# Optimization experiments

Measured on AMD Instinct MI355X. Metric: run time of the kernel, lower is better.

Reference implementation:

```python
import jax, jax.numpy as jnp
import numpy as np

EMBED = 128
HEADS = 32          # embed_dim // 4, forced by fuse Conv2d channel counts
HEAD_DIM = EMBED // HEADS  # 4
WS = (4, 7, 7)
N = WS[0] * WS[1] * WS[2]  # 196 tokens per window
B = 64              # batch * num_windows
SCALE = HEAD_DIM ** -0.5
EPS = 1e-5


def _rel_index():
    d, h, w = WS
    coords = np.stack(np.meshgrid(np.arange(d), np.arange(h), np.arange(w), indexing='ij'))
    flat = coords.reshape(3, -1)                       # [3, N]
    rel = (flat[:, :, None] - flat[:, None, :]).transpose(1, 2, 0).astype(np.int64)  # [N,N,3]
    rel[:, :, 0] += d - 1
    rel[:, :, 1] += h - 1
    rel[:, :, 2] += w - 1
    rel[:, :, 0] *= (2 * h - 1) * (2 * w - 1)
    rel[:, :, 1] *= (2 * w - 1)
    return rel.sum(-1).astype(np.int32)                # [N, N]


def setup_inputs() -> dict:
    key = jax.random.key(0)
    ks = jax.random.split(key, 7)
    d, h, w = WS
    tbl = (2 * d - 1) * (2 * h - 1) * (2 * w - 1)
    return {
        'x_in':      jax.random.normal(ks[0], (B, N, EMBED), dtype=jnp.float32),
        'x_in2':     jax.random.normal(ks[1], (B, N, EMBED), dtype=jnp.float32),
        'qkv_w':     jax.random.normal(ks[2], (3 * EMBED, EMBED), dtype=jnp.float32) * 0.02,
        'proj_w':    jax.random.normal(ks[3], (EMBED, EMBED), dtype=jnp.float32) * 0.02,
        'proj_b':    jnp.zeros((EMBED,), dtype=jnp.float32),
        'rpb_table': jax.random.normal(ks[4], (tbl, HEADS), dtype=jnp.float32) * 0.02,
        'fuse_w':    jax.random.normal(ks[5], (EMBED // 4, EMBED // 2), dtype=jnp.float32) * 0.1,
        'fuse_b':    jnp.zeros((EMBED // 4,), dtype=jnp.float32),
        'rel_idx':   jnp.asarray(_rel_index()),
    }


def _branch(x, qkv_w):
    b, n, c = x.shape
    qkv = (x @ qkv_w.T).reshape(b, n, 3, HEADS, c // HEADS).transpose(2, 0, 3, 1, 4)
    q, k, v = qkv[0] * SCALE, qkv[1], qkv[2]           # [b, H, n, d]
    attn = jnp.einsum('bhnd,bhmd->bhnm', q, k)         # [b, H, n, n]
    return attn, v


def reference(x_in, x_in2, qkv_w, proj_w, proj_b, rpb_table, fuse_w, fuse_b, rel_idx):
    b, n, c = x_in.shape
    attn1, v1 = _branch(x_in, qkv_w)
    attn2, v2 = _branch(x_in2, qkv_w)

    # conv-gated value fusion: Conv2d 1x1 over channel dim (= 2H) + InstanceNorm2d + ReLU + Sigmoid
    vcat = jnp.concatenate([v1, v2], axis=1)           # [b, 2H, n, d]
    v = jnp.einsum('bcnd,oc->bond', vcat, fuse_w) + fuse_b[None, :, None, None]  # [b, H, n, d]
    mu = v.mean(axis=(2, 3), keepdims=True)
    var = v.var(axis=(2, 3), keepdims=True)            # biased, as InstanceNorm2d
    v = (v - mu) * jax.lax.rsqrt(var + EPS)
    v = jax.nn.sigmoid(jax.nn.relu(v))

    # relative position bias: gather [n*n] rows of table -> [H, n, n]
    bias = rpb_table[rel_idx[:n, :n].reshape(-1)].reshape(n, n, HEADS).transpose(2, 0, 1)

    attn = jax.nn.softmax(attn1 + attn2 + bias[None], axis=-1)  # [b, H, n, n]
    x = jnp.einsum('bhnm,bhmd->bhnd', attn, v).transpose(0, 2, 1, 3).reshape(b, n, c)
    return x @ proj_w.T + proj_b
```

## Files before the change

kernel.cpp:

```cpp
#include <hip/hip_runtime.h>
#include <hip/hip_bf16.h>
#include <stdint.h>

#define NB   64
#define NTOK 196
#define NH   32
#define HD   4
#define CE   128
#define NM   38416

typedef __bf16 bf16x8 __attribute__((ext_vector_type(8)));
typedef short  bf16x4s __attribute__((ext_vector_type(4)));
typedef float  f32x4  __attribute__((ext_vector_type(4)));

#define QSCALE 0.7213475204444817f
#define LOG2E  1.4426950408889634f

__device__ __forceinline__ float u2f(unsigned short u) {
    union { unsigned int i; float f; } z;
    z.i = ((unsigned int)u) << 16;
    return z.f;
}
__device__ __forceinline__ unsigned short f2u(float f) {
    union { float f; unsigned int i; } z; z.f = f;
    unsigned int x = z.i;
    return (unsigned short)((x + 0x7fffu + ((x >> 16) & 1u)) >> 16);
}

extern "C" __global__ __launch_bounds__(256) void qkv_bias(
    const float* __restrict__ x1,
    const float* __restrict__ x2,
    const float* __restrict__ qkvw,
    const int* __restrict__ rel_idx, const float* __restrict__ rpb,
    unsigned short* __restrict__ Qb, unsigned short* __restrict__ Kb,
    unsigned short* __restrict__ V, unsigned short* __restrict__ biasM)
{
    __shared__ alignas(16) unsigned short AT[64][136];
    __shared__ alignas(16) unsigned short BT[64][136];
    const int tid = threadIdx.x;

    if (blockIdx.y == 6) {
        const int bx = blockIdx.x;
        const int qt = bx % 13, h = bx / 13;
        const int lane = tid & 63, wv = tid >> 6;
        const int quad = lane >> 4, tc = lane & 15;
        for (int nt = wv; nt < 14; nt += 4) {
            union { uint2 v; unsigned short s[4]; } e;
#pragma unroll
            for (int r = 0; r < 4; ++r) {
                int q   = qt * 16 + tc;
                int key = nt * 16 + quad * 4 + r;
                unsigned short u = 0xFF80;
                if (q < 196 && key < 196) {
                    int idx = rel_idx[q * 196 + key];
                    u = f2u(rpb[idx * 32 + h] * LOG2E);
                }
                e.s[r] = u;
            }
            unsigned int off = (((h * 13 + qt) * 7 + (nt >> 1)) * 64 + lane) * 8
                               + (nt & 1) * 4;
            *(uint2*)(biasM + off) = e.v;
        }
        return;
    }
    if (blockIdx.x >= 392) return;

    const int r0 = blockIdx.x * 64;
    const int j0 = blockIdx.y * 64;

    for (int idx = tid; idx < 2048; idx += 256) {
        int row = idx >> 5, k0 = (idx & 31) << 2;
        int r = r0 + row;
        const float* xp = (r >= 12544) ? x2 : x1;
        int rem = r - ((r >= 12544) ? 12544 : 0);
        float4 v = *(const float4*)&xp[rem * 128 + k0];
        ushort4 u; u.x = f2u(v.x); u.y = f2u(v.y); u.z = f2u(v.z); u.w = f2u(v.w);
        *(ushort4*)&AT[row][k0] = u;
    }
    for (int idx = tid; idx < 2048; idx += 256) {
        int row = idx >> 5, k0 = (idx & 31) << 2;
        float4 v = *(const float4*)&qkvw[(j0 + row) * 128 + k0];
        ushort4 u; u.x = f2u(v.x); u.y = f2u(v.y); u.z = f2u(v.z); u.w = f2u(v.w);
        *(ushort4*)&BT[row][k0] = u;
    }
    __syncthreads();

    const int lane = tid & 63, w = tid >> 6;
    const int wj = (w >> 1) * 32;
    const int wt = (w & 1) * 32;
    const int quad = lane >> 4, tc = lane & 15;

    f32x4 acc[2][2] = {};
#pragma unroll
    for (int ks = 0; ks < 4; ++ks) {
        int k0 = ks * 32 + quad * 8;
        bf16x8 a0 = *(const bf16x8*)&BT[wj + tc][k0];
        bf16x8 a1 = *(const bf16x8*)&BT[wj + 16 + tc][k0];
        bf16x8 b0 = *(const bf16x8*)&AT[wt + tc][k0];
        bf16x8 b1 = *(const bf16x8*)&AT[wt + 16 + tc][k0];
        acc[0][0] = __builtin_amdgcn_mfma_f32_16x16x32_bf16(a0, b0, acc[0][0], 0, 0, 0);
        acc[0][1] = __builtin_amdgcn_mfma_f32_16x16x32_bf16(a0, b1, acc[0][1], 0, 0, 0);
        acc[1][0] = __builtin_amdgcn_mfma_f32_16x16x32_bf16(a1, b0, acc[1][0], 0, 0, 0);
        acc[1][1] = __builtin_amdgcn_mfma_f32_16x16x32_bf16(a1, b1, acc[1][1], 0, 0, 0);
    }

    const int sel = j0 >> 7;
#pragma unroll
    for (int mi = 0; mi < 2; ++mi) {
        int jbase = (j0 + wj + mi * 16 + quad * 4) & 127;
        int hh = jbase >> 2;
#pragma unroll
        for (int ni = 0; ni < 2; ++ni) {
            int tok = r0 + wt + ni * 16 + tc;
            int branch = (tok >= 12544) ? 1 : 0;
            int rem = tok - branch * 12544;
            int bb = rem / 196;
            int nn = rem - bb * 196;
            union { uint2 v; unsigned short s[4]; } pk2;
            if (sel == 0) {
#pragma unroll
                for (int r = 0; r < 4; ++r) pk2.s[r] = f2u(acc[mi][ni][r] * QSCALE);
                *(uint2*)&Qb[((bb * 32 + hh) * 196 + nn) * 8 + branch * 4] = pk2.v;
            } else if (sel == 1) {
#pragma unroll
                for (int r = 0; r < 4; ++r) pk2.s[r] = f2u(acc[mi][ni][r]);
                *(uint2*)&Kb[((bb * 32 + hh) * 196 + nn) * 8 + branch * 4] = pk2.v;
            } else {
#pragma unroll
                for (int r = 0; r < 4; ++r) pk2.s[r] = f2u(acc[mi][ni][r]);
                *(uint2*)&V[(bb * 64 + branch * 32 + hh) * 784 + nn * 4] = pk2.v;
            }
        }
    }
}

__device__ __forceinline__ float block_sum(float v, float* red, int tid) {
#pragma unroll
    for (int off = 32; off > 0; off >>= 1) v += __shfl_down(v, off);
    __syncthreads();
    if ((tid & 63) == 0) red[tid >> 6] = v;
    __syncthreads();
    return red[0] + red[1] + red[2] + red[3];
}

__device__ __forceinline__ float act_sig_relu(float x) {
    return x > 0.f ? __fdividef(1.f, 1.f + __expf(-x)) : 0.5f;
}

extern "C" __global__ __launch_bounds__(256) void fuse_kernel(
    const unsigned short* __restrict__ V,
    const float* __restrict__ fuse_w,
    const float* __restrict__ fuse_b,
    float* __restrict__ Vf)
{
    const int b = blockIdx.x, o0 = blockIdx.y * 2;
    const int tid = threadIdx.x;
    __shared__ float fws[2][64];
    __shared__ float red[4];
    if (tid < 128) fws[tid >> 6][tid & 63] = fuse_w[(o0 + (tid >> 6)) * 64 + (tid & 63)];
    __syncthreads();

    const unsigned short* Vb = V + b * 64 * 784;
    float a0[3] = {0.f, 0.f, 0.f}, a1[3] = {0.f, 0.f, 0.f};
    float t0 = 0.f, t1 = 0.f;
    const bool tail = tid < 16;
    for (int c = 0; c < 64; ++c) {
        float w0 = fws[0][c], w1 = fws[1][c];
        const unsigned short* Vc = Vb + c * 784;
#pragma unroll
        for (int k = 0; k < 3; ++k) {
            float x = u2f(Vc[tid + 256 * k]);
            a0[k] = fmaf(w0, x, a0[k]);
            a1[k] = fmaf(w1, x, a1[k]);
        }
        if (tail) {
            float x = u2f(Vc[tid + 768]);
            t0 = fmaf(w0, x, t0);
            t1 = fmaf(w1, x, t1);
        }
    }
    float fb0 = fuse_b[o0], fb1 = fuse_b[o0 + 1];
#pragma unroll
    for (int k = 0; k < 3; ++k) { a0[k] += fb0; a1[k] += fb1; }
    t0 += fb0; t1 += fb1;

    float s0 = a0[0] + a0[1] + a0[2] + (tail ? t0 : 0.f);
    float q0 = a0[0]*a0[0] + a0[1]*a0[1] + a0[2]*a0[2] + (tail ? t0*t0 : 0.f);
    float s1 = a1[0] + a1[1] + a1[2] + (tail ? t1 : 0.f);
    float q1 = a1[0]*a1[0] + a1[1]*a1[1] + a1[2]*a1[2] + (tail ? t1*t1 : 0.f);

    float S0 = block_sum(s0, red, tid);
    float Q0 = block_sum(q0, red, tid);
    float S1 = block_sum(s1, red, tid);
    float Q1 = block_sum(q1, red, tid);

    const float inv = 1.0f / 784.0f;
    float mu0 = S0 * inv, mu1 = S1 * inv;
    float rs0 = rsqrtf(Q0 * inv - mu0 * mu0 + 1e-5f);
    float rs1 = rsqrtf(Q1 * inv - mu1 * mu1 + 1e-5f);

    float* out0 = Vf + (b * 32 + o0) * 784;
    float* out1 = out0 + 784;
#pragma unroll
    for (int k = 0; k < 3; ++k) {
        int e = tid + 256 * k;
        out0[e] = act_sig_relu((a0[k] - mu0) * rs0);
        out1[e] = act_sig_relu((a1[k] - mu1) * rs1);
    }
    if (tail) {
        out0[tid + 768] = act_sig_relu((t0 - mu0) * rs0);
        out1[tid + 768] = act_sig_relu((t1 - mu1) * rs1);
    }
}

extern "C" __global__ __launch_bounds__(256) void attn_kernel(
    const unsigned short* __restrict__ Qb, const unsigned short* __restrict__ Kb,
    const float* __restrict__ Vf, const unsigned short* __restrict__ biasM,
    unsigned short* __restrict__ Ob)
{
    const int bh = blockIdx.x;
    const int b = bh >> 5, h = bh & 31;
    __shared__ alignas(16) unsigned short Qs[208][8];
    __shared__ alignas(16) unsigned short Ks[224][8];
    __shared__ alignas(16) unsigned short VT[16][232];
    const int tid = threadIdx.x;

    const unsigned short* Qrow = Qb + bh * 196 * 8;
    const unsigned short* Krow = Kb + bh * 196 * 8;
    if (tid < 208) {
        uint4 z = {0, 0, 0, 0};
        uint4 v = (tid < 196) ? *(const uint4*)(Qrow + tid * 8) : z;
        *(uint4*)&Qs[tid][0] = v;
    }
    if (tid < 224) {
        uint4 z = {0, 0, 0, 0};
        uint4 v = (tid < 196) ? *(const uint4*)(Krow + tid * 8) : z;
        *(uint4*)&Ks[tid][0] = v;
    }
    {
        unsigned int* vtw = (unsigned int*)&VT[0][0];
        for (int i = tid; i < (16 * 232) / 2; i += 256) vtw[i] = 0u;
    }
    __syncthreads();
    if (tid < 196) {
        float4 vv = *(const float4*)(Vf + bh * 784 + tid * 4);
        VT[0][tid] = f2u(vv.x); VT[1][tid] = f2u(vv.y);
        VT[2][tid] = f2u(vv.z); VT[3][tid] = f2u(vv.w);
        VT[4][tid] = 0x3F80;
    }
    __syncthreads();

    const int lane = tid & 63, wv = tid >> 6;
    const int quad = lane >> 4, tc = lane & 15;

    bf16x4s vfr16[14];
#pragma unroll
    for (int t = 0; t < 14; ++t)
        vfr16[t] = *(const bf16x4s*)&VT[tc][t * 16 + quad * 4];

    const unsigned short* bias_h = biasM + (unsigned)(h * 13) * 3584;

    for (int qt = wv; qt < 13; qt += 4) {
        bf16x8 bq = {};
        if (quad == 0) bq = *(const bf16x8*)&Qs[qt * 16 + tc][0];
        const unsigned short* bias_q = bias_h + qt * 3584;
        f32x4 Oacc = {};
#pragma unroll
        for (int kt = 0; kt < 7; ++kt) {
            uint4 bw = *(const uint4*)(bias_q + kt * 512 + lane * 8);
            f32x4 s0, s1;
            {
                union { unsigned int u; float f; } c;
                c.u = bw.x << 16;          s0[0] = c.f;
                c.u = bw.x & 0xffff0000u;  s0[1] = c.f;
                c.u = bw.y << 16;          s0[2] = c.f;
                c.u = bw.y & 0xffff0000u;  s0[3] = c.f;
                c.u = bw.z << 16;          s1[0] = c.f;
                c.u = bw.z & 0xffff0000u;  s1[1] = c.f;
                c.u = bw.w << 16;          s1[2] = c.f;
                c.u = bw.w & 0xffff0000u;  s1[3] = c.f;
            }
            bf16x8 a0 = *(const bf16x8*)&Ks[(kt * 2 + 0) * 16 + tc][0];
            bf16x8 a1 = *(const bf16x8*)&Ks[(kt * 2 + 1) * 16 + tc][0];
            s0 = __builtin_amdgcn_mfma_f32_16x16x32_bf16(a0, bq, s0, 0, 0, 0);
            s1 = __builtin_amdgcn_mfma_f32_16x16x32_bf16(a1, bq, s1, 0, 0, 0);
            float e0 = __builtin_amdgcn_exp2f(s0[0]);
            float e1 = __builtin_amdgcn_exp2f(s0[1]);
            float e2 = __builtin_amdgcn_exp2f(s0[2]);
            float e3 = __builtin_amdgcn_exp2f(s0[3]);
            float g0 = __builtin_amdgcn_exp2f(s1[0]);
            float g1 = __builtin_amdgcn_exp2f(s1[1]);
            float g2 = __builtin_amdgcn_exp2f(s1[2]);
            float g3 = __builtin_amdgcn_exp2f(s1[3]);
            union { int d[2]; bf16x4s v; } pf0, pf1;
            pf0.d[0] = (int)__builtin_amdgcn_perm(__float_as_uint(e1), __float_as_uint(e0), 0x07060302u);
            pf0.d[1] = (int)__builtin_amdgcn_perm(__float_as_uint(e3), __float_as_uint(e2), 0x07060302u);
            pf1.d[0] = (int)__builtin_amdgcn_perm(__float_as_uint(g1), __float_as_uint(g0), 0x07060302u);
            pf1.d[1] = (int)__builtin_amdgcn_perm(__float_as_uint(g3), __float_as_uint(g2), 0x07060302u);
            Oacc = __builtin_amdgcn_mfma_f32_16x16x16bf16_1k(vfr16[kt * 2 + 0], pf0.v, Oacc, 0, 0, 0);
            Oacc = __builtin_amdgcn_mfma_f32_16x16x16bf16_1k(vfr16[kt * 2 + 1], pf1.v, Oacc, 0, 0, 0);
        }
        float rs = __shfl(Oacc[0], 16 + tc);
        int q = qt * 16 + tc;
        if (quad == 0 && q < 196) {
            float inv = __builtin_amdgcn_rcpf(rs);
            union { uint2 v; unsigned short s[4]; } pk2;
            pk2.s[0] = f2u(Oacc[0] * inv);
            pk2.s[1] = f2u(Oacc[1] * inv);
            pk2.s[2] = f2u(Oacc[2] * inv);
            pk2.s[3] = f2u(Oacc[3] * inv);
            *(uint2*)&Ob[(b * 196 + q) * 128 + h * 4] = pk2.v;
        }
    }
}

extern "C" __global__ __launch_bounds__(256) void proj_kernel(
    const unsigned short* __restrict__ Ob, const float* __restrict__ projw,
    const float* __restrict__ projb, float* __restrict__ out)
{
    __shared__ alignas(16) unsigned short AT[64][136];
    __shared__ alignas(16) unsigned short BT[64][136];
    const int tid = threadIdx.x;
    const int r0 = blockIdx.x * 64;
    const int j0 = blockIdx.y * 64;

    for (int idx = tid; idx < 1024; idx += 256) {
        int row = idx >> 4, k0 = (idx & 15) << 3;
        *(uint4*)&AT[row][k0] = *(const uint4*)&Ob[(r0 + row) * 128 + k0];
    }
    for (int idx = tid; idx < 2048; idx += 256) {
        int row = idx >> 5, k0 = (idx & 31) << 2;
        float4 v = *(const float4*)&projw[(j0 + row) * 128 + k0];
        ushort4 u; u.x = f2u(v.x); u.y = f2u(v.y); u.z = f2u(v.z); u.w = f2u(v.w);
        *(ushort4*)&BT[row][k0] = u;
    }
    __syncthreads();

    const int lane = tid & 63, w = tid >> 6;
    const int wm = (w >> 1) * 32, wn = (w & 1) * 32;
    const int quad = lane >> 4, tcol = lane & 15;

    f32x4 acc[2][2] = {};
#pragma unroll
    for (int ks = 0; ks < 4; ++ks) {
        int k0 = ks * 32 + quad * 8;
        bf16x8 a0 = *(const bf16x8*)&AT[wm + tcol][k0];
        bf16x8 a1 = *(const bf16x8*)&AT[wm + 16 + tcol][k0];
        bf16x8 b0 = *(const bf16x8*)&BT[wn + tcol][k0];
        bf16x8 b1 = *(const bf16x8*)&BT[wn + 16 + tcol][k0];
        acc[0][0] = __builtin_amdgcn_mfma_f32_16x16x32_bf16(a0, b0, acc[0][0], 0, 0, 0);
        acc[0][1] = __builtin_amdgcn_mfma_f32_16x16x32_bf16(a0, b1, acc[0][1], 0, 0, 0);
        acc[1][0] = __builtin_amdgcn_mfma_f32_16x16x32_bf16(a1, b0, acc[1][0], 0, 0, 0);
        acc[1][1] = __builtin_amdgcn_mfma_f32_16x16x32_bf16(a1, b1, acc[1][1], 0, 0, 0);
    }

#pragma unroll
    for (int mi = 0; mi < 2; ++mi) {
#pragma unroll
        for (int ni = 0; ni < 2; ++ni) {
            int j = j0 + wn + ni * 16 + tcol;
            float pb = projb[j];
#pragma unroll
            for (int reg = 0; reg < 4; ++reg) {
                int r = r0 + wm + mi * 16 + quad * 4 + reg;
                out[r * 128 + j] = acc[mi][ni][reg] + pb;
            }
        }
    }
}

extern "C" void kernel_launch(void* const* d_in, const int* in_sizes, int n_in,
                              void* d_out, int out_size, void* d_ws, size_t ws_size,
                              hipStream_t stream)
{
    const float* x1    = (const float*)d_in[0];
    const float* x2    = (const float*)d_in[1];
    const float* qkvw  = (const float*)d_in[2];
    const float* projw = (const float*)d_in[3];
    const float* projb = (const float*)d_in[4];
    const float* rpb   = (const float*)d_in[5];
    const float* fw    = (const float*)d_in[6];
    const float* fb    = (const float*)d_in[7];
    const int*   rel   = (const int*)d_in[8];
    float* out = (float*)d_out;

    char* w = (char*)d_ws;
    unsigned short* Qb  = (unsigned short*)(w);
    unsigned short* Kb  = (unsigned short*)(w + 6422528);
    unsigned short* V   = (unsigned short*)(w + 12845056);
    float*          Vf  = (float*)(w + 19267584);
    unsigned short* bM  = (unsigned short*)(w + 25690112);
    unsigned short* Ob  = (unsigned short*)(w + 28672000);

    qkv_bias  <<<dim3(416, 7), dim3(256), 0, stream>>>(x1, x2, qkvw, rel, rpb,
                                                       Qb, Kb, V, bM);
    fuse_kernel<<<dim3(64, 16), dim3(256), 0, stream>>>(V, fw, fb, Vf);
    attn_kernel<<<dim3(2048),   dim3(256), 0, stream>>>(Qb, Kb, Vf, bM, Ob);
    proj_kernel<<<dim3(196, 2), dim3(256), 0, stream>>>(Ob, projw, projb, out);
}
```

Baseline: 153.7 us.

## Fuse conv-gated value fusion into attention kernel and split PV accumulators

```diff
diff --git a/kernel.cpp b/kernel.cpp
--- a/kernel.cpp
+++ b/kernel.cpp
@@ -147,75 +147,10 @@
     return x > 0.f ? __fdividef(1.f, 1.f + __expf(-x)) : 0.5f;
 }
 
-extern "C" __global__ __launch_bounds__(256) void fuse_kernel(
-    const unsigned short* __restrict__ V,
-    const float* __restrict__ fuse_w,
-    const float* __restrict__ fuse_b,
-    float* __restrict__ Vf)
-{
-    const int b = blockIdx.x, o0 = blockIdx.y * 2;
-    const int tid = threadIdx.x;
-    __shared__ float fws[2][64];
-    __shared__ float red[4];
-    if (tid < 128) fws[tid >> 6][tid & 63] = fuse_w[(o0 + (tid >> 6)) * 64 + (tid & 63)];
-    __syncthreads();
-
-    const unsigned short* Vb = V + b * 64 * 784;
-    float a0[3] = {0.f, 0.f, 0.f}, a1[3] = {0.f, 0.f, 0.f};
-    float t0 = 0.f, t1 = 0.f;
-    const bool tail = tid < 16;
-    for (int c = 0; c < 64; ++c) {
-        float w0 = fws[0][c], w1 = fws[1][c];
-        const unsigned short* Vc = Vb + c * 784;
-#pragma unroll
-        for (int k = 0; k < 3; ++k) {
-            float x = u2f(Vc[tid + 256 * k]);
-            a0[k] = fmaf(w0, x, a0[k]);
-            a1[k] = fmaf(w1, x, a1[k]);
-        }
-        if (tail) {
-            float x = u2f(Vc[tid + 768]);
-            t0 = fmaf(w0, x, t0);
-            t1 = fmaf(w1, x, t1);
-        }
-    }
-    float fb0 = fuse_b[o0], fb1 = fuse_b[o0 + 1];
-#pragma unroll
-    for (int k = 0; k < 3; ++k) { a0[k] += fb0; a1[k] += fb1; }
-    t0 += fb0; t1 += fb1;
-
-    float s0 = a0[0] + a0[1] + a0[2] + (tail ? t0 : 0.f);
-    float q0 = a0[0]*a0[0] + a0[1]*a0[1] + a0[2]*a0[2] + (tail ? t0*t0 : 0.f);
-    float s1 = a1[0] + a1[1] + a1[2] + (tail ? t1 : 0.f);
-    float q1 = a1[0]*a1[0] + a1[1]*a1[1] + a1[2]*a1[2] + (tail ? t1*t1 : 0.f);
-
-    float S0 = block_sum(s0, red, tid);
-    float Q0 = block_sum(q0, red, tid);
-    float S1 = block_sum(s1, red, tid);
-    float Q1 = block_sum(q1, red, tid);
-
-    const float inv = 1.0f / 784.0f;
-    float mu0 = S0 * inv, mu1 = S1 * inv;
-    float rs0 = rsqrtf(Q0 * inv - mu0 * mu0 + 1e-5f);
-    float rs1 = rsqrtf(Q1 * inv - mu1 * mu1 + 1e-5f);
-
-    float* out0 = Vf + (b * 32 + o0) * 784;
-    float* out1 = out0 + 784;
-#pragma unroll
-    for (int k = 0; k < 3; ++k) {
-        int e = tid + 256 * k;
-        out0[e] = act_sig_relu((a0[k] - mu0) * rs0);
-        out1[e] = act_sig_relu((a1[k] - mu1) * rs1);
-    }
-    if (tail) {
-        out0[tid + 768] = act_sig_relu((t0 - mu0) * rs0);
-        out1[tid + 768] = act_sig_relu((t1 - mu1) * rs1);
-    }
-}
-
 extern "C" __global__ __launch_bounds__(256) void attn_kernel(
     const unsigned short* __restrict__ Qb, const unsigned short* __restrict__ Kb,
-    const float* __restrict__ Vf, const unsigned short* __restrict__ biasM,
+    const unsigned short* __restrict__ V, const float* __restrict__ fuse_w,
+    const float* __restrict__ fuse_b, const unsigned short* __restrict__ biasM,
     unsigned short* __restrict__ Ob)
 {
     const int bh = blockIdx.x;
@@ -223,6 +158,8 @@
     __shared__ alignas(16) unsigned short Qs[208][8];
     __shared__ alignas(16) unsigned short Ks[224][8];
     __shared__ alignas(16) unsigned short VT[16][232];
+    __shared__ float fws[64];
+    __shared__ float red[4];
     const int tid = threadIdx.x;
 
     const unsigned short* Qrow = Qb + bh * 196 * 8;
@@ -241,12 +178,47 @@
         unsigned int* vtw = (unsigned int*)&VT[0][0];
         for (int i = tid; i < (16 * 232) / 2; i += 256) vtw[i] = 0u;
     }
-    __syncthreads();
-    if (tid < 196) {
-        float4 vv = *(const float4*)(Vf + bh * 784 + tid * 4);
-        VT[0][tid] = f2u(vv.x); VT[1][tid] = f2u(vv.y);
-        VT[2][tid] = f2u(vv.z); VT[3][tid] = f2u(vv.w);
-        VT[4][tid] = 0x3F80;
+    if (tid < 64) fws[tid] = fuse_w[h * 64 + tid];
+    __syncthreads();
+
+    const unsigned short* Vb = V + b * 64 * 784;
+    float a0 = 0.f, a1 = 0.f, a2 = 0.f, t0 = 0.f;
+    const bool tail = tid < 16;
+    for (int c = 0; c < 64; ++c) {
+        float w0 = fws[c];
+        const unsigned short* Vc = Vb + c * 784;
+        a0 = fmaf(w0, u2f(Vc[tid]),       a0);
+        a1 = fmaf(w0, u2f(Vc[tid + 256]), a1);
+        a2 = fmaf(w0, u2f(Vc[tid + 512]), a2);
+        if (tail) t0 = fmaf(w0, u2f(Vc[tid + 768]), t0);
+    }
+    float fb0 = fuse_b[h];
+    a0 += fb0; a1 += fb0; a2 += fb0; t0 += fb0;
+
+    float s_  = a0 + a1 + a2 + (tail ? t0 : 0.f);
+    float q_  = a0*a0 + a1*a1 + a2*a2 + (tail ? t0*t0 : 0.f);
+    float S0 = block_sum(s_, red, tid);
+    float Q0 = block_sum(q_, red, tid);
+    const float inv784 = 1.0f / 784.0f;
+    float mu = S0 * inv784;
+    float rstd = rsqrtf(Q0 * inv784 - mu * mu + 1e-5f);
+
+    {
+        float vals[4] = { act_sig_relu((a0 - mu) * rstd),
+                          act_sig_relu((a1 - mu) * rstd),
+                          act_sig_relu((a2 - mu) * rstd),
+                          act_sig_relu((t0 - mu) * rstd) };
+#pragma unroll
+        for (int k = 0; k < 3; ++k) {
+            int nd = tid + 256 * k;
+            VT[nd & 3][nd >> 2] = f2u(vals[k]);
+            if ((nd & 3) == 0) VT[4][nd >> 2] = 0x3F80;
+        }
+        if (tail) {
+            int nd = tid + 768;
+            VT[nd & 3][nd >> 2] = f2u(vals[3]);
+            if ((nd & 3) == 0) VT[4][nd >> 2] = 0x3F80;
+        }
     }
     __syncthreads();
 
@@ -264,26 +236,29 @@
         bf16x8 bq = {};
         if (quad == 0) bq = *(const bf16x8*)&Qs[qt * 16 + tc][0];
         const unsigned short* bias_q = bias_h + qt * 3584;
-        f32x4 Oacc = {};
+        uint4 bw[7];
+#pragma unroll
+        for (int kt = 0; kt < 7; ++kt)
+            bw[kt] = *(const uint4*)(bias_q + kt * 512 + lane * 8);
+        f32x4 O0 = {}, O1 = {};
 #pragma unroll
         for (int kt = 0; kt < 7; ++kt) {
-            uint4 bw = *(const uint4*)(bias_q + kt * 512 + lane * 8);
             f32x4 s0, s1;
             {
                 union { unsigned int u; float f; } c;
-                c.u = bw.x << 16;          s0[0] = c.f;
-                c.u = bw.x & 0xffff0000u;  s0[1] = c.f;
-                c.u = bw.y << 16;          s0[2] = c.f;
-                c.u = bw.y & 0xffff0000u;  s0[3] = c.f;
-                c.u = bw.z << 16;          s1[0] = c.f;
-                c.u = bw.z & 0xffff0000u;  s1[1] = c.f;
-                c.u = bw.w << 16;          s1[2] = c.f;
-                c.u = bw.w & 0xffff0000u;  s1[3] = c.f;
+                c.u = bw[kt].x << 16;          s0[0] = c.f;
+                c.u = bw[kt].x & 0xffff0000u;  s0[1] = c.f;
+                c.u = bw[kt].y << 16;          s0[2] = c.f;
+                c.u = bw[kt].y & 0xffff0000u;  s0[3] = c.f;
+                c.u = bw[kt].z << 16;          s1[0] = c.f;
+                c.u = bw[kt].z & 0xffff0000u;  s1[1] = c.f;
+                c.u = bw[kt].w << 16;          s1[2] = c.f;
+                c.u = bw[kt].w & 0xffff0000u;  s1[3] = c.f;
             }
-            bf16x8 a0 = *(const bf16x8*)&Ks[(kt * 2 + 0) * 16 + tc][0];
-            bf16x8 a1 = *(const bf16x8*)&Ks[(kt * 2 + 1) * 16 + tc][0];
-            s0 = __builtin_amdgcn_mfma_f32_16x16x32_bf16(a0, bq, s0, 0, 0, 0);
-            s1 = __builtin_amdgcn_mfma_f32_16x16x32_bf16(a1, bq, s1, 0, 0, 0);
+            bf16x8 ka0 = *(const bf16x8*)&Ks[(kt * 2 + 0) * 16 + tc][0];
+            bf16x8 ka1 = *(const bf16x8*)&Ks[(kt * 2 + 1) * 16 + tc][0];
+            s0 = __builtin_amdgcn_mfma_f32_16x16x32_bf16(ka0, bq, s0, 0, 0, 0);
+            s1 = __builtin_amdgcn_mfma_f32_16x16x32_bf16(ka1, bq, s1, 0, 0, 0);
             float e0 = __builtin_amdgcn_exp2f(s0[0]);
             float e1 = __builtin_amdgcn_exp2f(s0[1]);
             float e2 = __builtin_amdgcn_exp2f(s0[2]);
@@ -297,9 +272,14 @@
             pf0.d[1] = (int)__builtin_amdgcn_perm(__float_as_uint(e3), __float_as_uint(e2), 0x07060302u);
             pf1.d[0] = (int)__builtin_amdgcn_perm(__float_as_uint(g1), __float_as_uint(g0), 0x07060302u);
             pf1.d[1] = (int)__builtin_amdgcn_perm(__float_as_uint(g3), __float_as_uint(g2), 0x07060302u);
-            Oacc = __builtin_amdgcn_mfma_f32_16x16x16bf16_1k(vfr16[kt * 2 + 0], pf0.v, Oacc, 0, 0, 0);
-            Oacc = __builtin_amdgcn_mfma_f32_16x16x16bf16_1k(vfr16[kt * 2 + 1], pf1.v, Oacc, 0, 0, 0);
-        }
+            O0 = __builtin_amdgcn_mfma_f32_16x16x16bf16_1k(vfr16[kt * 2 + 0], pf0.v, O0, 0, 0, 0);
+            O1 = __builtin_amdgcn_mfma_f32_16x16x16bf16_1k(vfr16[kt * 2 + 1], pf1.v, O1, 0, 0, 0);
+        }
+        f32x4 Oacc;
+        Oacc[0] = O0[0] + O1[0];
+        Oacc[1] = O0[1] + O1[1];
+        Oacc[2] = O0[2] + O1[2];
+        Oacc[3] = O0[3] + O1[3];
         float rs = __shfl(Oacc[0], 16 + tc);
         int q = qt * 16 + tc;
         if (quad == 0 && q < 196) {
@@ -388,13 +368,11 @@
     unsigned short* Qb  = (unsigned short*)(w);
     unsigned short* Kb  = (unsigned short*)(w + 6422528);
     unsigned short* V   = (unsigned short*)(w + 12845056);
-    float*          Vf  = (float*)(w + 19267584);
-    unsigned short* bM  = (unsigned short*)(w + 25690112);
-    unsigned short* Ob  = (unsigned short*)(w + 28672000);
+    unsigned short* bM  = (unsigned short*)(w + 19267584);
+    unsigned short* Ob  = (unsigned short*)(w + 22249472);
 
     qkv_bias  <<<dim3(416, 7), dim3(256), 0, stream>>>(x1, x2, qkvw, rel, rpb,
                                                        Qb, Kb, V, bM);
-    fuse_kernel<<<dim3(64, 16), dim3(256), 0, stream>>>(V, fw, fb, Vf);
-    attn_kernel<<<dim3(2048),   dim3(256), 0, stream>>>(Qb, Kb, Vf, bM, Ob);
+    attn_kernel<<<dim3(2048),   dim3(256), 0, stream>>>(Qb, Kb, V, fw, fb, bM, Ob);
     proj_kernel<<<dim3(196, 2), dim3(256), 0, stream>>>(Ob, projw, projb, out);
 }
```

Result: slower. 175.4 us (+14.1%).
